# Kernel optimization log

Hardware: AMD Instinct MI355X
Metric: run time of the kernel (lower is better)

Reference implementation:

```python
import jax, jax.numpy as jnp
import numpy as np
from jax import lax

K = 3          # kernel_size
STRIDE = 1
DN = ('NHWC', 'HWIO', 'NHWC')


def setup_inputs() -> dict:
    key = jax.random.key(0)
    k1, k2, k3 = jax.random.split(key, 3)
    inputs = jax.random.normal(k1, (8, 256, 256, 3), dtype=jnp.float32)
    # truncated-normal-ish init, stddev 0.1
    w_mu = 0.1 * jax.random.truncated_normal(k2, -2.0, 2.0, (K, K, 3, 128), dtype=jnp.float32)
    w_sigma = jax.random.uniform(k3, (128,), minval=-12.0, maxval=-4.6, dtype=jnp.float32)
    return {"inputs": inputs, "w_mu": w_mu, "w_sigma": w_sigma}


def reference(inputs, w_mu, w_sigma):
    # mean path: standard conv2d
    mu_out = lax.conv_general_dilated(inputs, w_mu, (STRIDE, STRIDE), 'VALID',
                                      dimension_numbers=DN)
    # variance path: original code does (x_patches**2) @ broadcast(softplus(w_sigma)).
    # Since vect_sigma is constant along the patch dimension, this equals
    # sum-over-patch(x^2) * softplus(w_sigma)[c]. Compute sum-pool via a ones conv,
    # avoiding materializing the huge im2col patch tensor.
    sp_sigma = jax.nn.softplus(w_sigma)                      # [Cout]
    cin = inputs.shape[-1]
    ones_k = jnp.ones((K, K, cin, 1), dtype=inputs.dtype)
    sumsq = lax.conv_general_dilated(inputs * inputs, ones_k, (STRIDE, STRIDE),
                                     'VALID', dimension_numbers=DN)  # [N,H',W',1]
    sigma_out = sumsq * sp_sigma                              # broadcast -> [N,H',W',Cout]
    return mu_out, sigma_out
```

## Files before the change

kernel.cpp:

```cpp
#include <hip/hip_runtime.h>
#include <hip/hip_fp16.h>
#include <math.h>

#define H_IN   256
#define W_IN   256
#define CIN    3
#define COUT   128
#define NB     8
#define KS     3
#define H_OUT  254
#define W_OUT  254
#define ROW_F  (W_IN * CIN)

#define FMA_MIX_LO(acc, wp, xv) \
    asm("v_fma_mix_f32 %0, %1, %2, %0 op_sel:[0,0,0] op_sel_hi:[1,0,0]" \
        : "+v"(acc) : "v"(wp), "v"(xv))
#define FMA_MIX_HI(acc, wp, xv) \
    asm("v_fma_mix_f32 %0, %1, %2, %0 op_sel:[1,0,0] op_sel_hi:[1,0,0]" \
        : "+v"(acc) : "v"(wp), "v"(xv))

__global__ __launch_bounds__(256, 4)
void conv_meanvar_kernel(const float* __restrict__ in,
                         const float* __restrict__ w_mu,
                         const float* __restrict__ w_sigma,
                         float* __restrict__ out)
{
    __shared__ float lds[3 * ROW_F + 32];

    const int h   = blockIdx.x;
    const int n   = blockIdx.y;
    const int tid = threadIdx.x;
    const int px  = tid >> 5;
    const int c4  = (tid & 31) * 4;

    const float* src = in + (size_t)(n * H_IN + h) * ROW_F;
    if (tid < 144) {
        const float4* s4 = reinterpret_cast<const float4*>(src) + tid * 4;
        float4* d4 = reinterpret_cast<float4*>(lds) + tid * 4;
        d4[0] = s4[0]; d4[1] = s4[1]; d4[2] = s4[2]; d4[3] = s4[3];
    }

    unsigned int wpk[27][2];
    #pragma unroll
    for (int kk = 0; kk < 27; ++kk) {
        float4 w = *reinterpret_cast<const float4*>(w_mu + kk * COUT + c4);
        wpk[kk][0] = (unsigned int)__half_as_ushort(__float2half(w.x))
                   | ((unsigned int)__half_as_ushort(__float2half(w.y)) << 16);
        wpk[kk][1] = (unsigned int)__half_as_ushort(__float2half(w.z))
                   | ((unsigned int)__half_as_ushort(__float2half(w.w)) << 16);
    }

    float4 ws = *reinterpret_cast<const float4*>(w_sigma + c4);
    float sp[4];
    sp[0] = log1pf(expf(ws.x));
    sp[1] = log1pf(expf(ws.y));
    sp[2] = log1pf(expf(ws.z));
    sp[3] = log1pf(expf(ws.w));

    __syncthreads();

    const size_t pix_base = (size_t)(n * H_OUT + h) * W_OUT;
    float* const out_sig  = out + (size_t)NB * H_OUT * W_OUT * COUT;

    #pragma unroll 1
    for (int it = 0; it < 8; ++it) {
        const int p0 = it * 32 + px * 4;

        float mu[4][4];
        float ss[4];
        #pragma unroll
        for (int j = 0; j < 4; ++j) {
            ss[j] = 0.f;
            mu[j][0] = mu[j][1] = mu[j][2] = mu[j][3] = 0.f;
        }

        #pragma unroll
        for (int kh = 0; kh < KS; ++kh) {
            const float4* rq = reinterpret_cast<const float4*>(
                                   &lds[kh * ROW_F + p0 * 3]);
            float r[20];
            *reinterpret_cast<float4*>(&r[0])  = rq[0];
            *reinterpret_cast<float4*>(&r[4])  = rq[1];
            *reinterpret_cast<float4*>(&r[8])  = rq[2];
            *reinterpret_cast<float4*>(&r[12]) = rq[3];
            *reinterpret_cast<float4*>(&r[16]) = rq[4];

            #pragma unroll
            for (int j = 0; j < 4; ++j) {
                #pragma unroll
                for (int q = 0; q < 9; ++q) {
                    const float x = r[j * 3 + q];
                    const int kk = kh * 9 + q;
                    FMA_MIX_LO(mu[j][0], wpk[kk][0], x);
                    FMA_MIX_HI(mu[j][1], wpk[kk][0], x);
                    FMA_MIX_LO(mu[j][2], wpk[kk][1], x);
                    FMA_MIX_HI(mu[j][3], wpk[kk][1], x);
                    ss[j] = fmaf(x, x, ss[j]);
                }
            }
        }

        #pragma unroll
        for (int j = 0; j < 4; ++j) {
            const int p = p0 + j;
            if (p < W_OUT) {
                const size_t o = (pix_base + p) * COUT + c4;
                float4 m = {mu[j][0], mu[j][1], mu[j][2], mu[j][3]};
                *reinterpret_cast<float4*>(out + o) = m;
                float4 sg = {ss[j] * sp[0], ss[j] * sp[1],
                             ss[j] * sp[2], ss[j] * sp[3]};
                *reinterpret_cast<float4*>(out_sig + o) = sg;
            }
        }
    }
}

extern "C" void kernel_launch(void* const* d_in, const int* in_sizes, int n_in,
                              void* d_out, int out_size, void* d_ws, size_t ws_size,
                              hipStream_t stream)
{
    const float* in      = (const float*)d_in[0];
    const float* w_mu    = (const float*)d_in[1];
    const float* w_sigma = (const float*)d_in[2];
    float* out           = (float*)d_out;

    dim3 grid(H_OUT, NB);
    dim3 block(256);
    conv_meanvar_kernel<<<grid, block, 0, stream>>>(in, w_mu, w_sigma, out);
}
```

Before: 114.5 us.

## Compute conv mean and sum-of-squares paths with f16 MFMA instructions

Replaces the per-thread VALU mixed-precision FMA loop with MFMA 16x16x16 f16 instructions. The 27-long patch is padded to 32 and the input row is staged as fp16 in shared memory. The sum of squares is computed by an MFMA against a ones vector and broadcast with a shuffle. Output writes become scalar 4-byte stores laid out by the MFMA accumulator format, which may coalesce less well than the previous float4 stores. Squaring inputs in fp16 also lowers precision on the variance path.

```diff
diff --git a/kernel.cpp b/kernel.cpp
--- a/kernel.cpp
+++ b/kernel.cpp
@@ -7,109 +7,111 @@
 #define CIN    3
 #define COUT   128
 #define NB     8
-#define KS     3
 #define H_OUT  254
 #define W_OUT  254
 #define ROW_F  (W_IN * CIN)
+#define XH_SZ  3328
 
-#define FMA_MIX_LO(acc, wp, xv) \
-    asm("v_fma_mix_f32 %0, %1, %2, %0 op_sel:[0,0,0] op_sel_hi:[1,0,0]" \
-        : "+v"(acc) : "v"(wp), "v"(xv))
-#define FMA_MIX_HI(acc, wp, xv) \
-    asm("v_fma_mix_f32 %0, %1, %2, %0 op_sel:[1,0,0] op_sel_hi:[1,0,0]" \
-        : "+v"(acc) : "v"(wp), "v"(xv))
+typedef _Float16 half4 __attribute__((ext_vector_type(4)));
+typedef float    f32x4 __attribute__((ext_vector_type(4)));
 
 __global__ __launch_bounds__(256, 4)
-void conv_meanvar_kernel(const float* __restrict__ in,
-                         const float* __restrict__ w_mu,
-                         const float* __restrict__ w_sigma,
-                         float* __restrict__ out)
+void conv_mfma_kernel(const float* __restrict__ in,
+                      const float* __restrict__ w_mu,
+                      const float* __restrict__ w_sigma,
+                      float* __restrict__ out)
 {
-    __shared__ float lds[3 * ROW_F + 32];
+    __shared__ _Float16 xh[XH_SZ];
 
-    const int h   = blockIdx.x;
-    const int n   = blockIdx.y;
-    const int tid = threadIdx.x;
-    const int px  = tid >> 5;
-    const int c4  = (tid & 31) * 4;
+    const int h    = blockIdx.x;
+    const int n    = blockIdx.y;
+    const int tid  = threadIdx.x;
+    const int lane = tid & 63;
+    const int wid  = tid >> 6;
+    const int g    = lane >> 4;
+    const int m    = lane & 15;
+
+    half4 bw[8][2];
+    #pragma unroll
+    for (int t = 0; t < 8; ++t) {
+        #pragma unroll
+        for (int hf = 0; hf < 2; ++hf) {
+            #pragma unroll
+            for (int j = 0; j < 4; ++j) {
+                const int k = g * 4 + j + 16 * hf;
+                const float w = (k < 27) ? w_mu[k * COUT + t * 16 + m] : 0.f;
+                bw[t][hf][j] = (_Float16)w;
+            }
+        }
+    }
+
+    half4 bones;
+    #pragma unroll
+    for (int j = 0; j < 4; ++j) bones[j] = (m == 0) ? (_Float16)1.f : (_Float16)0.f;
+
+    float sp[8];
+    #pragma unroll
+    for (int t = 0; t < 8; ++t) sp[t] = log1pf(expf(w_sigma[t * 16 + m]));
+
+    int offE[8];
+    #pragma unroll
+    for (int jh = 0; jh < 8; ++jh) {
+        const int k  = g * 4 + (jh & 3) + 16 * (jh >> 2);
+        const int kh = k / 9, r9 = k - kh * 9;
+        const int kw = r9 / 3, ci = r9 - kw * 3;
+        offE[jh] = kh * ROW_F + kw * CIN + ci;
+    }
 
     const float* src = in + (size_t)(n * H_IN + h) * ROW_F;
-    if (tid < 144) {
-        const float4* s4 = reinterpret_cast<const float4*>(src) + tid * 4;
-        float4* d4 = reinterpret_cast<float4*>(lds) + tid * 4;
-        d4[0] = s4[0]; d4[1] = s4[1]; d4[2] = s4[2]; d4[3] = s4[3];
-    }
-
-    unsigned int wpk[27][2];
-    #pragma unroll
-    for (int kk = 0; kk < 27; ++kk) {
-        float4 w = *reinterpret_cast<const float4*>(w_mu + kk * COUT + c4);
-        wpk[kk][0] = (unsigned int)__half_as_ushort(__float2half(w.x))
-                   | ((unsigned int)__half_as_ushort(__float2half(w.y)) << 16);
-        wpk[kk][1] = (unsigned int)__half_as_ushort(__float2half(w.z))
-                   | ((unsigned int)__half_as_ushort(__float2half(w.w)) << 16);
-    }
-
-    float4 ws = *reinterpret_cast<const float4*>(w_sigma + c4);
-    float sp[4];
-    sp[0] = log1pf(expf(ws.x));
-    sp[1] = log1pf(expf(ws.y));
-    sp[2] = log1pf(expf(ws.z));
-    sp[3] = log1pf(expf(ws.w));
-
+    for (int i = tid; i < XH_SZ; i += 256)
+        xh[i] = (i < 3 * ROW_F) ? (_Float16)src[i] : (_Float16)0.f;
     __syncthreads();
 
     const size_t pix_base = (size_t)(n * H_OUT + h) * W_OUT;
     float* const out_sig  = out + (size_t)NB * H_OUT * W_OUT * COUT;
 
     #pragma unroll 1
-    for (int it = 0; it < 8; ++it) {
-        const int p0 = it * 32 + px * 4;
+    for (int pass = 0; pass < 4; ++pass) {
+        const int pbase = pass * 64 + wid * 16;
+        const int p3    = (pbase + m) * 3;
 
-        float mu[4][4];
-        float ss[4];
+        half4 alo, ahi;
         #pragma unroll
-        for (int j = 0; j < 4; ++j) {
-            ss[j] = 0.f;
-            mu[j][0] = mu[j][1] = mu[j][2] = mu[j][3] = 0.f;
-        }
+        for (int j = 0; j < 4; ++j) alo[j] = xh[offE[j] + p3];
+        #pragma unroll
+        for (int j = 0; j < 4; ++j) ahi[j] = xh[offE[4 + j] + p3];
+
+        const half4 alo2 = alo * alo;
+        const half4 ahi2 = ahi * ahi;
+
+        const f32x4 z = {0.f, 0.f, 0.f, 0.f};
+        f32x4 acc[8];
+        #pragma unroll
+        for (int t = 0; t < 8; ++t) acc[t] = z;
+        f32x4 ssa = z;
 
         #pragma unroll
-        for (int kh = 0; kh < KS; ++kh) {
-            const float4* rq = reinterpret_cast<const float4*>(
-                                   &lds[kh * ROW_F + p0 * 3]);
-            float r[20];
-            *reinterpret_cast<float4*>(&r[0])  = rq[0];
-            *reinterpret_cast<float4*>(&r[4])  = rq[1];
-            *reinterpret_cast<float4*>(&r[8])  = rq[2];
-            *reinterpret_cast<float4*>(&r[12]) = rq[3];
-            *reinterpret_cast<float4*>(&r[16]) = rq[4];
+        for (int t = 0; t < 8; ++t) {
+            acc[t] = __builtin_amdgcn_mfma_f32_16x16x16f16(alo, bw[t][0], acc[t], 0, 0, 0);
+            acc[t] = __builtin_amdgcn_mfma_f32_16x16x16f16(ahi, bw[t][1], acc[t], 0, 0, 0);
+        }
+        ssa = __builtin_amdgcn_mfma_f32_16x16x16f16(alo2, bones, ssa, 0, 0, 0);
+        ssa = __builtin_amdgcn_mfma_f32_16x16x16f16(ahi2, bones, ssa, 0, 0, 0);
 
-            #pragma unroll
-            for (int j = 0; j < 4; ++j) {
-                #pragma unroll
-                for (int q = 0; q < 9; ++q) {
-                    const float x = r[j * 3 + q];
-                    const int kk = kh * 9 + q;
-                    FMA_MIX_LO(mu[j][0], wpk[kk][0], x);
-                    FMA_MIX_HI(mu[j][1], wpk[kk][0], x);
-                    FMA_MIX_LO(mu[j][2], wpk[kk][1], x);
-                    FMA_MIX_HI(mu[j][3], wpk[kk][1], x);
-                    ss[j] = fmaf(x, x, ss[j]);
-                }
-            }
-        }
+        float* const bmu = out     + (pix_base + pbase) * COUT;
+        float* const bsg = out_sig + (pix_base + pbase) * COUT;
+        const int vo = g * 4 * COUT + m;
 
         #pragma unroll
-        for (int j = 0; j < 4; ++j) {
-            const int p = p0 + j;
-            if (p < W_OUT) {
-                const size_t o = (pix_base + p) * COUT + c4;
-                float4 m = {mu[j][0], mu[j][1], mu[j][2], mu[j][3]};
-                *reinterpret_cast<float4*>(out + o) = m;
-                float4 sg = {ss[j] * sp[0], ss[j] * sp[1],
-                             ss[j] * sp[2], ss[j] * sp[3]};
-                *reinterpret_cast<float4*>(out_sig + o) = sg;
+        for (int r = 0; r < 4; ++r) {
+            const int q = pbase + g * 4 + r;
+            const float ssr = __shfl(ssa[r], lane & 48, 64);
+            if (q < W_OUT) {
+                #pragma unroll
+                for (int t = 0; t < 8; ++t) {
+                    bmu[vo + r * COUT + t * 16] = acc[t][r];
+                    bsg[vo + r * COUT + t * 16] = ssr * sp[t];
+                }
             }
         }
     }
@@ -126,5 +128,5 @@
 
     dim3 grid(H_OUT, NB);
     dim3 block(256);
-    conv_meanvar_kernel<<<grid, block, 0, stream>>>(in, w_mu, w_sigma, out);
+    conv_mfma_kernel<<<grid, block, 0, stream>>>(in, w_mu, w_sigma, out);
 }
```

New measurement: 125.2 us. 9.4% more time.
